# Performance work log

Measured on AMD Instinct MI355X. Metric: run time of the kernel, lower is better.

## Reference

```python
import jax, jax.numpy as jnp
import numpy as np

B, T, C = 4, 1024, 1024
H, HKV, D = 16, 4, 64
GATE_CH = 12
ROPE_THETA = 10000.0


def _rms_norm(x):
    # F.rms_norm with default eps = machine epsilon of dtype, no learnable scale
    eps = jnp.finfo(x.dtype).eps
    ms = jnp.mean(jnp.square(x), axis=-1, keepdims=True)
    return x * jax.lax.rsqrt(ms + eps)


def _apply_rotary(x, cos, sin):
    # x: (B, T, h, D); cos/sin: (1, T, 1, D//2). Half-split rotation.
    d = x.shape[-1] // 2
    x1, x2 = x[..., :d], x[..., d:]
    y1 = x1 * cos + x2 * sin
    y2 = -x1 * sin + x2 * cos
    return jnp.concatenate([y1, y2], axis=-1)


def setup_inputs() -> dict:
    key = jax.random.key(0)
    ks = jax.random.split(key, 8)
    x = jax.random.normal(ks[0], (B, T, C), dtype=jnp.float32)
    ve = jax.random.normal(ks[1], (B, T, HKV * D), dtype=jnp.float32)
    # real RoPE tables, shape (1, T, 1, D//2)
    half = D // 2
    inv_freq = 1.0 / (ROPE_THETA ** (np.arange(half, dtype=np.float32) / half))
    freqs = np.arange(T, dtype=np.float32)[:, None] * inv_freq[None, :]
    cos = jnp.asarray(np.cos(freqs), dtype=jnp.float32).reshape(1, T, 1, half)
    sin = jnp.asarray(np.sin(freqs), dtype=jnp.float32).reshape(1, T, 1, half)
    s = 0.02
    Wq = jax.random.normal(ks[2], (H * D, C), dtype=jnp.float32) * s
    Wk = jax.random.normal(ks[3], (HKV * D, C), dtype=jnp.float32) * s
    Wv = jax.random.normal(ks[4], (HKV * D, C), dtype=jnp.float32) * s
    Wo = jax.random.normal(ks[5], (C, C), dtype=jnp.float32) * s
    Wg = jax.random.normal(ks[6], (HKV, GATE_CH), dtype=jnp.float32) * s
    return {"x": x, "ve": ve, "cos": cos, "sin": sin,
            "Wq": Wq, "Wk": Wk, "Wv": Wv, "Wo": Wo, "Wg": Wg,
            "window_size": 256}


def reference(x, ve, cos, sin, Wq, Wk, Wv, Wo, Wg, window_size):
    b, t, c = x.shape
    d = 2 * cos.shape[-1]
    h = Wq.shape[0] // d
    hkv = Wk.shape[0] // d
    rep = h // hkv

    q = (x @ Wq.T).reshape(b, t, h, d)
    k = (x @ Wk.T).reshape(b, t, hkv, d)
    v = (x @ Wv.T).reshape(b, t, hkv, d)

    # value-embedding sigmoid gate (3 * sigmoid of first 12 channels of x)
    gate = 3.0 * jax.nn.sigmoid(x[..., : Wg.shape[1]] @ Wg.T)  # (b, t, hkv)
    v = v + gate[..., None] * ve.reshape(b, t, hkv, d)

    q = _apply_rotary(q, cos, sin)
    k = _apply_rotary(k, cos, sin)
    q = _rms_norm(q) * 1.2
    k = _rms_norm(k) * 1.2

    # GQA attention with sliding-window causal mask (left=window_size, right=0)
    qg = q.reshape(b, t, hkv, rep, d)
    scale = 1.0 / jnp.sqrt(jnp.asarray(d, dtype=q.dtype))
    scores = jnp.einsum('bqgrd,bkgd->bgrqk', qg, k) * scale
    i = jnp.arange(t)[:, None]
    j = jnp.arange(t)[None, :]
    mask = (j <= i) & ((i - j) <= window_size)  # (t, t)
    scores = jnp.where(mask[None, None, None], scores, -jnp.inf)
    probs = jax.nn.softmax(scores, axis=-1)
    y = jnp.einsum('bgrqk,bkgd->bqgrd', probs, v).reshape(b, t, h * d)
    return y @ Wo.T
```

## Files before the change

kernel.cpp:

```cpp
#include <hip/hip_runtime.h>

typedef __bf16 v8bf __attribute__((ext_vector_type(8)));
typedef float v4f __attribute__((ext_vector_type(4)));
typedef unsigned int v4u __attribute__((ext_vector_type(4)));
typedef unsigned int v2u __attribute__((ext_vector_type(2)));
typedef unsigned short u16;

#define DEVI static __device__ __forceinline__

DEVI float bf2f(u16 u) {
    union { float f; unsigned int i; } c; c.i = ((unsigned int)u) << 16; return c.f;
}
DEVI u16 f2bf(float f) {
    union { float f; unsigned int i; } c; c.f = f;
    unsigned int i = c.i;
    i += 0x7fffu + ((i >> 16) & 1u);
    return (u16)(i >> 16);
}

union Frag { v4u u; v8bf v; u16 h[8]; };

#define GLD16(gptr, lptr) __builtin_amdgcn_global_load_lds( \
    (const __attribute__((address_space(1))) void*)(gptr),  \
    (__attribute__((address_space(3))) void*)(lptr), 16, 0, 0)

__global__ __launch_bounds__(256) void convert5(
    const float* __restrict__ x, const float* __restrict__ wq,
    const float* __restrict__ wk, const float* __restrict__ wv,
    const float* __restrict__ wo, u16* __restrict__ xb,
    u16* __restrict__ wb, u16* __restrict__ wob)
{
    const float* src; u16* dst; int n;
    switch (blockIdx.y) {
        case 0: src = x;  dst = xb;               n = 4096 * 1024; break;
        case 1: src = wq; dst = wb;               n = 1024 * 1024; break;
        case 2: src = wk; dst = wb + 1024 * 1024; n = 256 * 1024;  break;
        case 3: src = wv; dst = wb + 1280 * 1024; n = 256 * 1024;  break;
        default: src = wo; dst = wob;             n = 1024 * 1024; break;
    }
    const int stride = gridDim.x * 256 * 4;
    for (int i = (blockIdx.x * 256 + threadIdx.x) * 4; i < n; i += stride) {
        const float4 f = *(const float4*)(src + i);
        v2u p;
        p[0] = (unsigned int)f2bf(f.x) | ((unsigned int)f2bf(f.y) << 16);
        p[1] = (unsigned int)f2bf(f.z) | ((unsigned int)f2bf(f.w) << 16);
        *(v2u*)(dst + i) = p;
    }
}

template <bool F32OUT>
__global__ __launch_bounds__(256) void gemm_bt(
    const u16* __restrict__ A, const u16* __restrict__ B,
    void* __restrict__ Cv, int N)
{
    __shared__ __align__(16) u16 As[64 * 64];
    __shared__ __align__(16) u16 Bs[128 * 64];
    const int tid  = threadIdx.x;
    const int lane = tid & 63, l15 = lane & 15, quad = lane >> 4;
    const int w    = tid >> 6;
    const int wr   = (w >> 1) * 32, wc = (w & 1) * 64;
    const int m0   = blockIdx.y * 64, n0 = blockIdx.x * 128;

    const u16* ab = A + m0 * 1024;
    const u16* bb = B + n0 * 1024;

    const int r0 = tid >> 3;
    const int c0 = (tid & 7) * 8;
    const u16* ag = ab + r0 * 1024 + c0;
    const u16* bg = bb + r0 * 1024 + c0;
    u16* al = &As[r0 * 64 + c0];
    u16* bl = &Bs[r0 * 64 + c0];

    v4f acc[2][4];
    const v4f vzero = {0.f, 0.f, 0.f, 0.f};
#pragma unroll
    for (int i = 0; i < 2; i++)
#pragma unroll
        for (int j = 0; j < 4; j++) acc[i][j] = vzero;

    for (int k0 = 0; k0 < 1024; k0 += 64) {
        __syncthreads();
        GLD16(ag + k0,             al);
        GLD16(ag + k0 + 32 * 1024, al + 32 * 64);
        GLD16(bg + k0,             bl);
        GLD16(bg + k0 + 32 * 1024, bl + 32 * 64);
        GLD16(bg + k0 + 64 * 1024, bl + 64 * 64);
        GLD16(bg + k0 + 96 * 1024, bl + 96 * 64);
        __syncthreads();
#pragma unroll
        for (int ks = 0; ks < 2; ks++) {
            v8bf af[2];
#pragma unroll
            for (int mi = 0; mi < 2; mi++)
                af[mi] = *(const v8bf*)&As[(wr + mi * 16 + l15) * 64 + ks * 32 + quad * 8];
#pragma unroll
            for (int ni = 0; ni < 4; ni++) {
                v8bf bv = *(const v8bf*)&Bs[(wc + ni * 16 + l15) * 64 + ks * 32 + quad * 8];
#pragma unroll
                for (int mi = 0; mi < 2; mi++)
                    acc[mi][ni] = __builtin_amdgcn_mfma_f32_16x16x32_bf16(af[mi], bv, acc[mi][ni], 0, 0, 0);
            }
        }
    }
#pragma unroll
    for (int mi = 0; mi < 2; mi++) {
        const int row = m0 + wr + mi * 16 + quad * 4;
#pragma unroll
        for (int ni = 0; ni < 4; ni++) {
            const int col = n0 + wc + ni * 16 + l15;
#pragma unroll
            for (int r = 0; r < 4; r++) {
                if (F32OUT) ((float*)Cv)[(row + r) * N + col] = acc[mi][ni][r];
                else        ((u16*)Cv)[(row + r) * N + col] = f2bf(acc[mi][ni][r]);
            }
        }
    }
}

__global__ __launch_bounds__(256) void fixup(
    const u16* __restrict__ qkv, const float* __restrict__ x,
    const float* __restrict__ ve, const float* __restrict__ cs,
    const float* __restrict__ sn, const float* __restrict__ Wg,
    u16* __restrict__ qn, u16* __restrict__ kn, u16* __restrict__ vn)
{
    const int token = blockIdx.x;
    const int pos   = token & 1023;
    const int tid   = threadIdx.x;
    const int hw    = tid >> 5, l = tid & 31;
    const float c = cs[pos * 32 + l];
    const float s = sn[pos * 32 + l];
#pragma unroll
    for (int it = 0; it < 3; it++) {
        const int task = it * 8 + hw;
        if (task < 20) {
            const u16* src; u16* dst;
            if (task < 16) { src = qkv + token * 1536 + task * 64;               dst = qn + token * 1024 + task * 64; }
            else           { src = qkv + token * 1536 + 1024 + (task - 16) * 64; dst = kn + token * 256 + (task - 16) * 64; }
            const float x1 = bf2f(src[l]), x2 = bf2f(src[32 + l]);
            const float y1 = x1 * c + x2 * s;
            const float y2 = x2 * c - x1 * s;
            float ss = y1 * y1 + y2 * y2;
#pragma unroll
            for (int off = 16; off >= 1; off >>= 1) ss += __shfl_xor(ss, off, 64);
            const float inv = rsqrtf(ss * (1.0f / 64.0f) + 1.1920929e-7f) * 1.2f;
            dst[l]      = f2bf(y1 * inv);
            dst[32 + l] = f2bf(y2 * inv);
        } else {
            const int g = task - 20;
            float dot = 0.f;
#pragma unroll
            for (int cc = 0; cc < 12; cc++)
                dot += x[token * 1024 + cc] * Wg[g * 12 + cc];
            const float gate = 3.f / (1.f + __expf(-dot));
            const u16*   vsrc  = qkv + token * 1536 + 1280 + g * 64;
            const float* vesrc = ve + token * 256 + g * 64;
            u16* vdst = vn + token * 256 + g * 64;
            vdst[l]      = f2bf(bf2f(vsrc[l])      + gate * vesrc[l]);
            vdst[32 + l] = f2bf(bf2f(vsrc[32 + l]) + gate * vesrc[32 + l]);
        }
    }
}

__global__ __launch_bounds__(256) void vtrans(
    const u16* __restrict__ vn, u16* __restrict__ vt)
{
    __shared__ __align__(16) u16 T[64 * 72];
    const int tid = threadIdx.x;
    const int t0  = blockIdx.x * 64, g = blockIdx.y, b = blockIdx.z;
    {
        const int row = tid >> 2, ch = (tid & 3) * 16;
        const int goff = (b * 1024 + t0 + row) * 256 + g * 64 + ch;
        *(v4u*)&T[row * 72 + ch]     = *(const v4u*)&vn[goff];
        *(v4u*)&T[row * 72 + ch + 8] = *(const v4u*)&vn[goff + 8];
    }
    __syncthreads();
    {
        const int d = tid >> 2, tc = (tid & 3) * 16;
        Frag o0, o1;
#pragma unroll
        for (int j = 0; j < 8; j++) {
            o0.h[j] = T[(tc + j) * 72 + d];
            o1.h[j] = T[(tc + 8 + j) * 72 + d];
        }
        u16* dst = vt + ((b * 4 + g) * 64 + d) * 1024 + t0 + tc;
        *(v4u*)dst       = o0.u;
        *(v4u*)(dst + 8) = o1.u;
    }
}

__global__ __launch_bounds__(256) void attn(
    const u16* __restrict__ qn, const u16* __restrict__ kn,
    const u16* __restrict__ vt, u16* __restrict__ yo)
{
    __shared__ __align__(16) u16 Ks[64 * 72];
    __shared__ __align__(16) u16 VTs[64 * 72];
    __shared__ __align__(16) u16 Ps[4][16 * 72];
    const int tid  = threadIdx.x;
    const int w    = tid >> 6, lane = tid & 63, l15 = lane & 15, quad = lane >> 4;
    const int qb   = blockIdx.x, h = blockIdx.y, b = blockIdx.z;
    const int g    = h >> 2;
    const int qbase = qb * 64;
    const int qabs0 = qbase + w * 16;
    const int tok0  = b * 1024 + qabs0;
    u16* pw = Ps[w];

    v8bf qf[2];
#pragma unroll
    for (int ks = 0; ks < 2; ks++) {
        Frag f;
        f.u = *(const v4u*)&qn[(tok0 + l15) * 1024 + h * 64 + ks * 32 + quad * 8];
#pragma unroll
        for (int j = 0; j < 8; j++) f.h[j] = f2bf(0.125f * bf2f(f.h[j]));
        qf[ks] = f.v;
    }

    v4f o[4];
    float mi_[4], li_[4];
    const v4f vzero = {0.f, 0.f, 0.f, 0.f};
#pragma unroll
    for (int nd = 0; nd < 4; nd++) o[nd] = vzero;
#pragma unroll
    for (int r = 0; r < 4; r++) { mi_[r] = -1e30f; li_[r] = 0.f; }

    const int kstart = (qbase >= 256) ? qbase - 256 : 0;
    for (int kbase = kstart; kbase <= qbase; kbase += 64) {
        __syncthreads();
        {
            const int row = tid >> 2, ch = (tid & 3) * 16;
            const int goff = (b * 1024 + kbase + row) * 256 + g * 64 + ch;
            *(v4u*)&Ks[row * 72 + ch]     = *(const v4u*)&kn[goff];
            *(v4u*)&Ks[row * 72 + ch + 8] = *(const v4u*)&kn[goff + 8];
            const u16* vsrc = vt + ((b * 4 + g) * 64 + row) * 1024 + kbase + ch;
            *(v4u*)&VTs[row * 72 + ch]     = *(const v4u*)vsrc;
            *(v4u*)&VTs[row * 72 + ch + 8] = *(const v4u*)(vsrc + 8);
        }
        __syncthreads();

        bool skip[4], full[4];
#pragma unroll
        for (int ni = 0; ni < 4; ni++) {
            const int left = kbase + ni * 16;
            skip[ni] = (left > qabs0 + 15) || (qabs0 - (left + 15) > 256);
            full[ni] = ((left + 15) <= qabs0) && ((qabs0 + 15 - left) <= 256);
        }

        v4f sc[4];
        float rmax[4] = {-1e30f, -1e30f, -1e30f, -1e30f};
#pragma unroll
        for (int ni = 0; ni < 4; ni++) {
            if (skip[ni]) continue;
            v8bf kf0 = *(const v8bf*)&Ks[(ni * 16 + l15) * 72 + quad * 8];
            v8bf kf1 = *(const v8bf*)&Ks[(ni * 16 + l15) * 72 + 32 + quad * 8];
            v4f a = vzero;
            a = __builtin_amdgcn_mfma_f32_16x16x32_bf16(qf[0], kf0, a, 0, 0, 0);
            a = __builtin_amdgcn_mfma_f32_16x16x32_bf16(qf[1], kf1, a, 0, 0, 0);
            if (!full[ni]) {
                const int kj = kbase + ni * 16 + l15;
#pragma unroll
                for (int r = 0; r < 4; r++) {
                    const int qi = qabs0 + quad * 4 + r;
                    if (!((kj <= qi) && (qi - kj <= 256))) a[r] = -1e30f;
                }
            }
            sc[ni] = a;
#pragma unroll
            for (int r = 0; r < 4; r++) rmax[r] = fmaxf(rmax[r], a[r]);
        }
#pragma unroll
        for (int off = 8; off >= 1; off >>= 1)
#pragma unroll
            for (int r = 0; r < 4; r++)
                rmax[r] = fmaxf(rmax[r], __shfl_xor(rmax[r], off, 64));

        float mn[4], alp[4], ps[4];
#pragma unroll
        for (int r = 0; r < 4; r++) {
            mn[r]  = fmaxf(mi_[r], rmax[r]);
            alp[r] = __expf(mi_[r] - mn[r]);
            mi_[r] = mn[r];
            ps[r]  = 0.f;
        }
#pragma unroll
        for (int ni = 0; ni < 4; ni++) {
            if (skip[ni]) {
#pragma unroll
                for (int r = 0; r < 4; r++)
                    pw[(quad * 4 + r) * 72 + ni * 16 + l15] = 0;
            } else {
#pragma unroll
                for (int r = 0; r < 4; r++) {
                    const float p = __expf(sc[ni][r] - mn[r]);
                    ps[r] += p;
                    pw[(quad * 4 + r) * 72 + ni * 16 + l15] = f2bf(p);
                }
            }
        }
#pragma unroll
        for (int off = 8; off >= 1; off >>= 1)
#pragma unroll
            for (int r = 0; r < 4; r++)
                ps[r] += __shfl_xor(ps[r], off, 64);
#pragma unroll
        for (int r = 0; r < 4; r++)
            li_[r] = li_[r] * alp[r] + ps[r];
#pragma unroll
        for (int nd = 0; nd < 4; nd++)
#pragma unroll
            for (int r = 0; r < 4; r++)
                o[nd][r] *= alp[r];

#pragma unroll
        for (int ks = 0; ks < 2; ks++) {
            if (skip[2 * ks] && skip[2 * ks + 1]) continue;
            v8bf af = *(const v8bf*)&pw[l15 * 72 + ks * 32 + quad * 8];
#pragma unroll
            for (int nd = 0; nd < 4; nd++) {
                v8bf bv = *(const v8bf*)&VTs[(nd * 16 + l15) * 72 + ks * 32 + quad * 8];
                o[nd] = __builtin_amdgcn_mfma_f32_16x16x32_bf16(af, bv, o[nd], 0, 0, 0);
            }
        }
    }

    float inv[4];
#pragma unroll
    for (int r = 0; r < 4; r++) inv[r] = 1.f / li_[r];
#pragma unroll
    for (int nd = 0; nd < 4; nd++) {
        const int col = h * 64 + nd * 16 + l15;
#pragma unroll
        for (int r = 0; r < 4; r++) {
            const int row = tok0 + quad * 4 + r;
            yo[row * 1024 + col] = f2bf(o[nd][r] * inv[r]);
        }
    }
}

extern "C" void kernel_launch(void* const* d_in, const int* in_sizes, int n_in,
                              void* d_out, int out_size, void* d_ws, size_t ws_size,
                              hipStream_t stream)
{
    const float* x  = (const float*)d_in[0];
    const float* ve = (const float*)d_in[1];
    const float* cs = (const float*)d_in[2];
    const float* sn = (const float*)d_in[3];
    const float* Wq = (const float*)d_in[4];
    const float* Wk = (const float*)d_in[5];
    const float* Wv = (const float*)d_in[6];
    const float* Wo = (const float*)d_in[7];
    const float* Wg = (const float*)d_in[8];

    u16* xb  = (u16*)d_ws;
    u16* wb  = xb  + 4096 * 1024;
    u16* wob = wb  + 1536 * 1024;
    u16* qkv = wob + 1024 * 1024;
    u16* qn  = qkv + 4096 * 1536;
    u16* kn  = qn  + 4096 * 1024;
    u16* vn  = kn  + 4096 * 256;
    u16* vt  = vn  + 4096 * 256;
    u16* ay  = qkv;

    convert5<<<dim3(512, 5), 256, 0, stream>>>(x, Wq, Wk, Wv, Wo, xb, wb, wob);
    gemm_bt<false><<<dim3(12, 64), 256, 0, stream>>>(xb, wb, (void*)qkv, 1536);
    fixup<<<4096, 256, 0, stream>>>(qkv, x, ve, cs, sn, Wg, qn, kn, vn);
    vtrans<<<dim3(16, 4, 4), 256, 0, stream>>>(vn, vt);
    attn<<<dim3(16, 16, 4), 256, 0, stream>>>(qn, kn, vt, ay);
    gemm_bt<true><<<dim3(8, 64), 256, 0, stream>>>(ay, wob, d_out, 1024);
}
```

Baseline: 173.1 us.

## Fuse V transpose into fixup, enlarge attention q-tile, drop online softmax rescaling

Merges the fixup and V-transpose kernels so gated V is staged in shared memory and written transposed directly, removing the intermediate vn buffer and one launch. The attention kernel now gives each wave 32 query rows (128 per block), halving the grid and reusing each K/V tile across more queries. It also drops the running-max online softmax and uses a fixed offset of 12 in the exponent, which relies on scores being bounded by the RMS-normed q/k scale; this removes the per-tile max reductions and rescaling at the risk of overflow or underflow if that bound does not hold.

```diff
diff --git a/kernel.cpp b/kernel.cpp
--- a/kernel.cpp
+++ b/kernel.cpp
@@ -56,14 +56,13 @@
     __shared__ __align__(16) u16 As[64 * 64];
     __shared__ __align__(16) u16 Bs[128 * 64];
     const int tid  = threadIdx.x;
-    const int lane = tid & 63, l15 = lane & 15, quad = lane >> 4;
+    const int lane = tid & 63, l15 = lane & 15, quad = (lane >> 4) & 3;
     const int w    = tid >> 6;
     const int wr   = (w >> 1) * 32, wc = (w & 1) * 64;
     const int m0   = blockIdx.y * 64, n0 = blockIdx.x * 128;
 
     const u16* ab = A + m0 * 1024;
     const u16* bb = B + n0 * 1024;
-
     const int r0 = tid >> 3;
     const int c0 = (tid & 7) * 8;
     const u16* ag = ab + r0 * 1024 + c0;
@@ -117,74 +116,60 @@
     }
 }
 
-__global__ __launch_bounds__(256) void fixup(
+__global__ __launch_bounds__(256) void fixup_vt(
     const u16* __restrict__ qkv, const float* __restrict__ x,
     const float* __restrict__ ve, const float* __restrict__ cs,
     const float* __restrict__ sn, const float* __restrict__ Wg,
-    u16* __restrict__ qn, u16* __restrict__ kn, u16* __restrict__ vn)
-{
-    const int token = blockIdx.x;
-    const int pos   = token & 1023;
-    const int tid   = threadIdx.x;
-    const int hw    = tid >> 5, l = tid & 31;
-    const float c = cs[pos * 32 + l];
-    const float s = sn[pos * 32 + l];
-#pragma unroll
-    for (int it = 0; it < 3; it++) {
-        const int task = it * 8 + hw;
-        if (task < 20) {
-            const u16* src; u16* dst;
-            if (task < 16) { src = qkv + token * 1536 + task * 64;               dst = qn + token * 1024 + task * 64; }
-            else           { src = qkv + token * 1536 + 1024 + (task - 16) * 64; dst = kn + token * 256 + (task - 16) * 64; }
-            const float x1 = bf2f(src[l]), x2 = bf2f(src[32 + l]);
-            const float y1 = x1 * c + x2 * s;
-            const float y2 = x2 * c - x1 * s;
-            float ss = y1 * y1 + y2 * y2;
-#pragma unroll
-            for (int off = 16; off >= 1; off >>= 1) ss += __shfl_xor(ss, off, 64);
-            const float inv = rsqrtf(ss * (1.0f / 64.0f) + 1.1920929e-7f) * 1.2f;
-            dst[l]      = f2bf(y1 * inv);
-            dst[32 + l] = f2bf(y2 * inv);
-        } else {
-            const int g = task - 20;
-            float dot = 0.f;
-#pragma unroll
-            for (int cc = 0; cc < 12; cc++)
-                dot += x[token * 1024 + cc] * Wg[g * 12 + cc];
-            const float gate = 3.f / (1.f + __expf(-dot));
-            const u16*   vsrc  = qkv + token * 1536 + 1280 + g * 64;
-            const float* vesrc = ve + token * 256 + g * 64;
-            u16* vdst = vn + token * 256 + g * 64;
-            vdst[l]      = f2bf(bf2f(vsrc[l])      + gate * vesrc[l]);
-            vdst[32 + l] = f2bf(bf2f(vsrc[32 + l]) + gate * vesrc[32 + l]);
-        }
-    }
-}
-
-__global__ __launch_bounds__(256) void vtrans(
-    const u16* __restrict__ vn, u16* __restrict__ vt)
-{
-    __shared__ __align__(16) u16 T[64 * 72];
+    u16* __restrict__ qn, u16* __restrict__ kn, u16* __restrict__ vt)
+{
+    __shared__ __align__(16) u16 vbuf[2048];
     const int tid = threadIdx.x;
-    const int t0  = blockIdx.x * 64, g = blockIdx.y, b = blockIdx.z;
-    {
-        const int row = tid >> 2, ch = (tid & 3) * 16;
-        const int goff = (b * 1024 + t0 + row) * 256 + g * 64 + ch;
-        *(v4u*)&T[row * 72 + ch]     = *(const v4u*)&vn[goff];
-        *(v4u*)&T[row * 72 + ch + 8] = *(const v4u*)&vn[goff + 8];
+    const int token0 = blockIdx.x * 8;
+    const int b = token0 >> 10;
+    const int hw = tid >> 5, l = tid & 31;
+    for (int ti = 0; ti < 8; ti++) {
+        const int token = token0 + ti;
+        const int pos   = token & 1023;
+        const float c = cs[pos * 32 + l];
+        const float s = sn[pos * 32 + l];
+#pragma unroll
+        for (int it = 0; it < 3; it++) {
+            const int task = it * 8 + hw;
+            if (task < 20) {
+                const u16* src; u16* dst;
+                if (task < 16) { src = qkv + token * 1536 + task * 64;               dst = qn + token * 1024 + task * 64; }
+                else           { src = qkv + token * 1536 + 1024 + (task - 16) * 64; dst = kn + token * 256 + (task - 16) * 64; }
+                const float x1 = bf2f(src[l]), x2 = bf2f(src[32 + l]);
+                const float y1 = x1 * c + x2 * s;
+                const float y2 = x2 * c - x1 * s;
+                float ss = y1 * y1 + y2 * y2;
+#pragma unroll
+                for (int off = 16; off >= 1; off >>= 1) ss += __shfl_xor(ss, off, 64);
+                const float inv = rsqrtf(ss * (1.0f / 64.0f) + 1.1920929e-7f) * 1.2f;
+                dst[l]      = f2bf(y1 * inv);
+                dst[32 + l] = f2bf(y2 * inv);
+            } else {
+                const int g = task - 20;
+                float dot = 0.f;
+#pragma unroll
+                for (int cc = 0; cc < 12; cc++)
+                    dot += x[token * 1024 + cc] * Wg[g * 12 + cc];
+                const float gate = 3.f / (1.f + __expf(-dot));
+                const u16*   vsrc  = qkv + token * 1536 + 1280 + g * 64;
+                const float* vesrc = ve + token * 256 + g * 64;
+                vbuf[ti * 256 + g * 64 + l]      = f2bf(bf2f(vsrc[l])      + gate * vesrc[l]);
+                vbuf[ti * 256 + g * 64 + 32 + l] = f2bf(bf2f(vsrc[32 + l]) + gate * vesrc[32 + l]);
+            }
+        }
     }
     __syncthreads();
     {
-        const int d = tid >> 2, tc = (tid & 3) * 16;
-        Frag o0, o1;
-#pragma unroll
-        for (int j = 0; j < 8; j++) {
-            o0.h[j] = T[(tc + j) * 72 + d];
-            o1.h[j] = T[(tc + 8 + j) * 72 + d];
-        }
-        u16* dst = vt + ((b * 4 + g) * 64 + d) * 1024 + t0 + tc;
-        *(v4u*)dst       = o0.u;
-        *(v4u*)(dst + 8) = o1.u;
+        const int g = tid >> 6, d = tid & 63;
+        Frag f;
+#pragma unroll
+        for (int j = 0; j < 8; j++) f.h[j] = vbuf[j * 256 + tid];
+        u16* dst = vt + ((b * 4 + g) * 64 + d) * 1024 + (token0 & 1023);
+        *(v4u*)dst = f.u;
     }
 }
 
@@ -194,36 +179,42 @@
 {
     __shared__ __align__(16) u16 Ks[64 * 72];
     __shared__ __align__(16) u16 VTs[64 * 72];
-    __shared__ __align__(16) u16 Ps[4][16 * 72];
+    __shared__ __align__(16) u16 Ps[4][32 * 72];
     const int tid  = threadIdx.x;
-    const int w    = tid >> 6, lane = tid & 63, l15 = lane & 15, quad = lane >> 4;
+    const int w    = tid >> 6, lane = tid & 63, l15 = lane & 15, quad = (lane >> 4) & 3;
     const int qb   = blockIdx.x, h = blockIdx.y, b = blockIdx.z;
     const int g    = h >> 2;
-    const int qbase = qb * 64;
-    const int qabs0 = qbase + w * 16;
+    const int qbase = qb * 128;
+    const int qabs0 = qbase + w * 32;
     const int tok0  = b * 1024 + qabs0;
     u16* pw = Ps[w];
 
-    v8bf qf[2];
-#pragma unroll
-    for (int ks = 0; ks < 2; ks++) {
-        Frag f;
-        f.u = *(const v4u*)&qn[(tok0 + l15) * 1024 + h * 64 + ks * 32 + quad * 8];
-#pragma unroll
-        for (int j = 0; j < 8; j++) f.h[j] = f2bf(0.125f * bf2f(f.h[j]));
-        qf[ks] = f.v;
-    }
-
-    v4f o[4];
-    float mi_[4], li_[4];
+    v8bf qf[2][2];
+#pragma unroll
+    for (int mi = 0; mi < 2; mi++)
+#pragma unroll
+        for (int ks = 0; ks < 2; ks++) {
+            Frag f;
+            f.u = *(const v4u*)&qn[(tok0 + mi * 16 + l15) * 1024 + h * 64 + ks * 32 + quad * 8];
+#pragma unroll
+            for (int j = 0; j < 8; j++) f.h[j] = f2bf(0.125f * bf2f(f.h[j]));
+            qf[mi][ks] = f.v;
+        }
+
+    v4f o[2][4];
+    float li[2][4];
     const v4f vzero = {0.f, 0.f, 0.f, 0.f};
 #pragma unroll
-    for (int nd = 0; nd < 4; nd++) o[nd] = vzero;
-#pragma unroll
-    for (int r = 0; r < 4; r++) { mi_[r] = -1e30f; li_[r] = 0.f; }
+    for (int mi = 0; mi < 2; mi++) {
+#pragma unroll
+        for (int nd = 0; nd < 4; nd++) o[mi][nd] = vzero;
+#pragma unroll
+        for (int r = 0; r < 4; r++) li[mi][r] = 0.f;
+    }
 
     const int kstart = (qbase >= 256) ? qbase - 256 : 0;
-    for (int kbase = kstart; kbase <= qbase; kbase += 64) {
+    const int kend   = qbase + 64;
+    for (int kbase = kstart; kbase <= kend; kbase += 64) {
         __syncthreads();
         {
             const int row = tid >> 2, ch = (tid & 3) * 16;
@@ -236,101 +227,81 @@
         }
         __syncthreads();
 
-        bool skip[4], full[4];
-#pragma unroll
-        for (int ni = 0; ni < 4; ni++) {
-            const int left = kbase + ni * 16;
-            skip[ni] = (left > qabs0 + 15) || (qabs0 - (left + 15) > 256);
-            full[ni] = ((left + 15) <= qabs0) && ((qabs0 + 15 - left) <= 256);
-        }
-
-        v4f sc[4];
-        float rmax[4] = {-1e30f, -1e30f, -1e30f, -1e30f};
-#pragma unroll
-        for (int ni = 0; ni < 4; ni++) {
-            if (skip[ni]) continue;
-            v8bf kf0 = *(const v8bf*)&Ks[(ni * 16 + l15) * 72 + quad * 8];
-            v8bf kf1 = *(const v8bf*)&Ks[(ni * 16 + l15) * 72 + 32 + quad * 8];
-            v4f a = vzero;
-            a = __builtin_amdgcn_mfma_f32_16x16x32_bf16(qf[0], kf0, a, 0, 0, 0);
-            a = __builtin_amdgcn_mfma_f32_16x16x32_bf16(qf[1], kf1, a, 0, 0, 0);
-            if (!full[ni]) {
-                const int kj = kbase + ni * 16 + l15;
+        bool skip2[2][4], full2[2][4];
+#pragma unroll
+        for (int mi = 0; mi < 2; mi++)
+#pragma unroll
+            for (int ni = 0; ni < 4; ni++) {
+                const int qw = qabs0 + mi * 16;
+                const int left = kbase + ni * 16;
+                skip2[mi][ni] = (left > qw + 15) || (qw - (left + 15) > 256);
+                full2[mi][ni] = ((left + 15) <= qw) && ((qw + 15 - left) <= 256);
+            }
+
+#pragma unroll
+        for (int mi = 0; mi < 2; mi++) {
+#pragma unroll
+            for (int ni = 0; ni < 4; ni++) {
+                if (skip2[mi][ni]) {
+#pragma unroll
+                    for (int r = 0; r < 4; r++)
+                        pw[(mi * 16 + quad * 4 + r) * 72 + ni * 16 + l15] = 0;
+                    continue;
+                }
+                v8bf kf0 = *(const v8bf*)&Ks[(ni * 16 + l15) * 72 + quad * 8];
+                v8bf kf1 = *(const v8bf*)&Ks[(ni * 16 + l15) * 72 + 32 + quad * 8];
+                v4f a = vzero;
+                a = __builtin_amdgcn_mfma_f32_16x16x32_bf16(qf[mi][0], kf0, a, 0, 0, 0);
+                a = __builtin_amdgcn_mfma_f32_16x16x32_bf16(qf[mi][1], kf1, a, 0, 0, 0);
+                if (!full2[mi][ni]) {
+                    const int kj = kbase + ni * 16 + l15;
+#pragma unroll
+                    for (int r = 0; r < 4; r++) {
+                        const int qi = qabs0 + mi * 16 + quad * 4 + r;
+                        if (!((kj <= qi) && (qi - kj <= 256))) a[r] = -1e30f;
+                    }
+                }
 #pragma unroll
                 for (int r = 0; r < 4; r++) {
-                    const int qi = qabs0 + quad * 4 + r;
-                    if (!((kj <= qi) && (qi - kj <= 256))) a[r] = -1e30f;
+                    const float p = __expf(a[r] - 12.0f);
+                    li[mi][r] += p;
+                    pw[(mi * 16 + quad * 4 + r) * 72 + ni * 16 + l15] = f2bf(p);
                 }
             }
-            sc[ni] = a;
-#pragma unroll
-            for (int r = 0; r < 4; r++) rmax[r] = fmaxf(rmax[r], a[r]);
-        }
+        }
+
+#pragma unroll
+        for (int mi = 0; mi < 2; mi++)
+#pragma unroll
+            for (int ks = 0; ks < 2; ks++) {
+                if (skip2[mi][2 * ks] && skip2[mi][2 * ks + 1]) continue;
+                v8bf af = *(const v8bf*)&pw[(mi * 16 + l15) * 72 + ks * 32 + quad * 8];
+#pragma unroll
+                for (int nd = 0; nd < 4; nd++) {
+                    v8bf bv = *(const v8bf*)&VTs[(nd * 16 + l15) * 72 + ks * 32 + quad * 8];
+                    o[mi][nd] = __builtin_amdgcn_mfma_f32_16x16x32_bf16(af, bv, o[mi][nd], 0, 0, 0);
+                }
+            }
+    }
+
+#pragma unroll
+    for (int mi = 0; mi < 2; mi++) {
 #pragma unroll
         for (int off = 8; off >= 1; off >>= 1)
 #pragma unroll
             for (int r = 0; r < 4; r++)
-                rmax[r] = fmaxf(rmax[r], __shfl_xor(rmax[r], off, 64));
-
-        float mn[4], alp[4], ps[4];
-#pragma unroll
-        for (int r = 0; r < 4; r++) {
-            mn[r]  = fmaxf(mi_[r], rmax[r]);
-            alp[r] = __expf(mi_[r] - mn[r]);
-            mi_[r] = mn[r];
-            ps[r]  = 0.f;
-        }
-#pragma unroll
-        for (int ni = 0; ni < 4; ni++) {
-            if (skip[ni]) {
-#pragma unroll
-                for (int r = 0; r < 4; r++)
-                    pw[(quad * 4 + r) * 72 + ni * 16 + l15] = 0;
-            } else {
-#pragma unroll
-                for (int r = 0; r < 4; r++) {
-                    const float p = __expf(sc[ni][r] - mn[r]);
-                    ps[r] += p;
-                    pw[(quad * 4 + r) * 72 + ni * 16 + l15] = f2bf(p);
-                }
-            }
-        }
-#pragma unroll
-        for (int off = 8; off >= 1; off >>= 1)
-#pragma unroll
-            for (int r = 0; r < 4; r++)
-                ps[r] += __shfl_xor(ps[r], off, 64);
-#pragma unroll
-        for (int r = 0; r < 4; r++)
-            li_[r] = li_[r] * alp[r] + ps[r];
-#pragma unroll
-        for (int nd = 0; nd < 4; nd++)
-#pragma unroll
-            for (int r = 0; r < 4; r++)
-                o[nd][r] *= alp[r];
-
-#pragma unroll
-        for (int ks = 0; ks < 2; ks++) {
-            if (skip[2 * ks] && skip[2 * ks + 1]) continue;
-            v8bf af = *(const v8bf*)&pw[l15 * 72 + ks * 32 + quad * 8];
-#pragma unroll
-            for (int nd = 0; nd < 4; nd++) {
-                v8bf bv = *(const v8bf*)&VTs[(nd * 16 + l15) * 72 + ks * 32 + quad * 8];
-                o[nd] = __builtin_amdgcn_mfma_f32_16x16x32_bf16(af, bv, o[nd], 0, 0, 0);
-            }
-        }
-    }
-
-    float inv[4];
-#pragma unroll
-    for (int r = 0; r < 4; r++) inv[r] = 1.f / li_[r];
-#pragma unroll
-    for (int nd = 0; nd < 4; nd++) {
-        const int col = h * 64 + nd * 16 + l15;
-#pragma unroll
-        for (int r = 0; r < 4; r++) {
-            const int row = tok0 + quad * 4 + r;
-            yo[row * 1024 + col] = f2bf(o[nd][r] * inv[r]);
+                li[mi][r] += __shfl_xor(li[mi][r], off, 64);
+        float inv[4];
+#pragma unroll
+        for (int r = 0; r < 4; r++) inv[r] = 1.f / li[mi][r];
+#pragma unroll
+        for (int nd = 0; nd < 4; nd++) {
+            const int col = h * 64 + nd * 16 + l15;
+#pragma unroll
+            for (int r = 0; r < 4; r++) {
+                const int row = tok0 + mi * 16 + quad * 4 + r;
+                yo[row * 1024 + col] = f2bf(o[mi][nd][r] * inv[r]);
+            }
         }
     }
 }
@@ -355,14 +326,12 @@
     u16* qkv = wob + 1024 * 1024;
     u16* qn  = qkv + 4096 * 1536;
     u16* kn  = qn  + 4096 * 1024;
-    u16* vn  = kn  + 4096 * 256;
-    u16* vt  = vn  + 4096 * 256;
+    u16* vt  = kn  + 4096 * 256;
     u16* ay  = qkv;
 
     convert5<<<dim3(512, 5), 256, 0, stream>>>(x, Wq, Wk, Wv, Wo, xb, wb, wob);
     gemm_bt<false><<<dim3(12, 64), 256, 0, stream>>>(xb, wb, (void*)qkv, 1536);
-    fixup<<<4096, 256, 0, stream>>>(qkv, x, ve, cs, sn, Wg, qn, kn, vn);
-    vtrans<<<dim3(16, 4, 4), 256, 0, stream>>>(vn, vt);
-    attn<<<dim3(16, 16, 4), 256, 0, stream>>>(qn, kn, vt, ay);
+    fixup_vt<<<512, 256, 0, stream>>>(qkv, x, ve, cs, sn, Wg, qn, kn, vt);
+    attn<<<dim3(8, 16, 4), 256, 0, stream>>>(qn, kn, vt, ay);
     gemm_bt<true><<<dim3(8, 64), 256, 0, stream>>>(ay, wob, d_out, 1024);
 }
```

Measured after the change: 179.2 us. 1.04x slower.
